# Optimization experiments

Measured on AMD Instinct MI355X. Metric: run time of the kernel, lower is better.

The kernel has to match this reference:

```python
import jax, jax.numpy as jnp
import numpy as np

B, S, D = 4, 4096, 2048

def setup_inputs() -> dict:
    key = jax.random.key(0)
    k1, k2 = jax.random.split(key)
    k = jax.random.normal(k1, (B, S, D), dtype=jnp.float32)
    v = jax.random.normal(k2, (B, S, D), dtype=jnp.float32)
    kv_state = jnp.zeros((D, D), dtype=jnp.float32)
    k_sum = jnp.zeros((D,), dtype=jnp.float32)
    return {"k": k, "v": v, "kv_state": kv_state, "k_sum": k_sum}

def reference(k, v, kv_state, k_sum):
    b, s, d = k.shape
    k_flat = k.reshape(-1, d)  # (N, D), N = B*S
    v_flat = v.reshape(-1, d)
    # Accumulate outer-product state: kv_state += sum_i k_i v_i^T
    kv_new = kv_state + jnp.einsum('nd,ne->de', k_flat, v_flat)
    ks_new = k_sum + k_flat.sum(axis=0)
    # Readout: context = k @ kv_state^T ; normalizer = k @ k_sum
    context = jnp.einsum('nd,ed->ne', k_flat, kv_new).reshape(b, s, d)
    normalizer = (k_flat @ ks_new).reshape(b, s, 1)
    return context, normalizer
```

## Files before the change

### kernel.cpp

```cpp
#include <hip/hip_runtime.h>
#include <hip/hip_bf16.h>
#include <cstdio>
#include <cstdint>

#define NBIG 16384
#define DDIM 2048
#define SPLITK 4

#define BM 256
#define BN 256
#define BKT 64

typedef __attribute__((ext_vector_type(4))) float f32x4;
typedef __attribute__((ext_vector_type(8))) short bf16x8;

__device__ __forceinline__ unsigned short f2bf(float f) {
  union { float f; unsigned u; } v; v.f = f;
  return (unsigned short)((v.u + 0x7FFFu + ((v.u >> 16) & 1u)) >> 16);
}

__device__ __forceinline__ void gll16(const void* g, void* l) {
  auto gp = reinterpret_cast<const __attribute__((address_space(1))) unsigned int*>(
      reinterpret_cast<uintptr_t>(g));
  auto lp = reinterpret_cast<__attribute__((address_space(3))) unsigned int*>(
      (unsigned int)reinterpret_cast<uintptr_t>(l));
  __builtin_amdgcn_global_load_lds(gp, lp, 16, 0, 0);
}

__device__ __forceinline__ void waitvm8() { asm volatile("s_waitcnt vmcnt(8)" ::: "memory"); }
__device__ __forceinline__ void waitvm0() { asm volatile("s_waitcnt vmcnt(0)" ::: "memory"); }
__device__ __forceinline__ void barrier_pinned() {
  __builtin_amdgcn_sched_barrier(0);
  __builtin_amdgcn_s_barrier();
  __builtin_amdgcn_sched_barrier(0);
}

__device__ __forceinline__ void xcd_swizzle(int& bx, int& by, int& bz) {
  const unsigned nx = gridDim.x, ny = gridDim.y;
  const unsigned nwg = nx * ny * gridDim.z;
  unsigned wg = blockIdx.x + nx * (blockIdx.y + ny * blockIdx.z);
  wg = (wg & 7u) * (nwg >> 3) + (wg >> 3);
  bx = wg % nx;
  unsigned r = wg / nx;
  by = r % ny;
  bz = r / ny;
}

__global__ __launch_bounds__(256) void prep_kernel(
    const float* __restrict__ k, const float* __restrict__ v,
    unsigned short* __restrict__ KT, unsigned short* __restrict__ VT,
    unsigned short* __restrict__ Kbf, float* __restrict__ ks)
{
  __shared__ unsigned short sm[64][66];
  __shared__ float sks[64];
  const int t = threadIdx.x;
  const int tiles_d = DDIM / 64;
  const int n0 = (blockIdx.x / tiles_d) * 64;
  const int d0 = (blockIdx.x % tiles_d) * 64;
  const bool is_k = (blockIdx.y == 0);
  const float* __restrict__ src = is_k ? k : v;
  unsigned short* __restrict__ dstT = is_k ? KT : VT;

  const int r = t >> 4;
  const int c = (t & 15) * 4;

  if (t < 64) sks[t] = 0.f;
  __syncthreads();

  float a0 = 0.f, a1 = 0.f, a2 = 0.f, a3 = 0.f;
#pragma unroll
  for (int i = 0; i < 4; ++i) {
    const int row = i * 16 + r;
    f32x4 val = *reinterpret_cast<const f32x4*>(&src[(size_t)(n0 + row) * DDIM + d0 + c]);
    unsigned short b0 = f2bf(val.x), b1 = f2bf(val.y), b2 = f2bf(val.z), b3 = f2bf(val.w);
    sm[row][c + 0] = b0; sm[row][c + 1] = b1;
    sm[row][c + 2] = b2; sm[row][c + 3] = b3;
    if (is_k) {
      unsigned int p0 = (unsigned)b0 | ((unsigned)b1 << 16);
      unsigned int p1 = (unsigned)b2 | ((unsigned)b3 << 16);
      *reinterpret_cast<uint2*>(&Kbf[(size_t)(n0 + row) * DDIM + d0 + c]) = make_uint2(p0, p1);
      a0 += val.x; a1 += val.y; a2 += val.z; a3 += val.w;
    }
  }
  if (is_k) {
    atomicAdd(&sks[c + 0], a0);
    atomicAdd(&sks[c + 1], a1);
    atomicAdd(&sks[c + 2], a2);
    atomicAdd(&sks[c + 3], a3);
  }
  __syncthreads();

#pragma unroll
  for (int i = 0; i < 4; ++i) {
    const int rowp = i * 16 + r;
    unsigned int p0 = (unsigned)sm[c + 0][rowp] | ((unsigned)sm[c + 1][rowp] << 16);
    unsigned int p1 = (unsigned)sm[c + 2][rowp] | ((unsigned)sm[c + 3][rowp] << 16);
    *reinterpret_cast<uint2*>(&dstT[(size_t)(d0 + rowp) * NBIG + n0 + c]) = make_uint2(p0, p1);
  }
  if (is_k && t < 64) atomicAdd(&ks[d0 + t], sks[t]);
}

__global__ void init_ks_kernel(const float* __restrict__ ksum, float* __restrict__ ks) {
  int i = blockIdx.x * 256 + threadIdx.x;
  if (i < DDIM) ks[i] = ksum[i];
}

template <bool BF16OUT>
__global__ __launch_bounds__(512, 2) void gemm256_kernel(
    const unsigned short* __restrict__ A, const unsigned short* __restrict__ B,
    void* __restrict__ Cv, int lda, int ldb, int kchunk, long long zstride)
{
  __shared__ unsigned short Abuf[2][BM * BKT];
  __shared__ unsigned short Bbuf[2][BN * BKT];

  int bx, by, bz;
  xcd_swizzle(bx, by, bz);

  const int t = threadIdx.x, lane = t & 63, w = t >> 6;
  const int wm = w >> 2, wn = w & 3;
  const int m0 = by * BM, n0 = bx * BN;
  const int kbeg = bz * kchunk;
  const int NT = kchunk / BKT;

  const int srow = lane >> 3;
  const int sgr  = (lane & 7) ^ srow;
  const unsigned short* Ag = A + (size_t)(m0 + srow) * lda + kbeg + sgr * 8;
  const unsigned short* Bg = B + (size_t)(n0 + srow) * ldb + kbeg + sgr * 8;

  const int hi = lane >> 4;
  const int lo7 = lane & 7;
  const int swz0 = ((0 + hi) ^ lo7) * 8;
  const int swz1 = ((4 + hi) ^ lo7) * 8;
  const int arow = (wm * 128 + (lane & 15)) * BKT;
  const int brow = (wn * 64 + (lane & 15)) * BKT;

  auto stage_op = [&](const unsigned short* G, unsigned short* Lbase, int ld_,
                      int kt, int half) {
    const unsigned short* g = G + (size_t)(half * 128 + w * 16) * ld_ + (size_t)kt * BKT;
    unsigned short* l = Lbase + (half * 128 + w * 16) * BKT;
    gll16(g, l);
    gll16(g + (size_t)8 * ld_, l + 8 * BKT);
  };

  stage_op(Bg, Bbuf[0], ldb, 0, 0); stage_op(Bg, Bbuf[0], ldb, 0, 1);
  stage_op(Ag, Abuf[0], lda, 0, 0); stage_op(Ag, Abuf[0], lda, 0, 1);
  stage_op(Bg, Bbuf[1], ldb, 1, 0); stage_op(Bg, Bbuf[1], ldb, 1, 1);
  stage_op(Ag, Abuf[1], lda, 1, 0); stage_op(Ag, Abuf[1], lda, 1, 1);
  waitvm8();
  __builtin_amdgcn_s_barrier();
  __builtin_amdgcn_sched_barrier(0);

  f32x4 acc[8][4] = {};

#pragma unroll 2
  for (int tl = 0; tl < NT; ++tl) {
    const int q = tl & 1;
    const unsigned short* Al = Abuf[q];
    const unsigned short* Bl = Bbuf[q];
    bf16x8 af[4][2], bA[2][2], bB[2][2];

#pragma unroll
    for (int m = 0; m < 4; ++m) {
      af[m][0] = *reinterpret_cast<const bf16x8*>(Al + arow + m * 16 * BKT + swz0);
      af[m][1] = *reinterpret_cast<const bf16x8*>(Al + arow + m * 16 * BKT + swz1);
    }
#pragma unroll
    for (int n = 0; n < 2; ++n) {
      bA[n][0] = *reinterpret_cast<const bf16x8*>(Bl + brow + n * 16 * BKT + swz0);
      bA[n][1] = *reinterpret_cast<const bf16x8*>(Bl + brow + n * 16 * BKT + swz1);
    }
    __builtin_amdgcn_s_setprio(1);
#pragma unroll
    for (int kk = 0; kk < 2; ++kk)
#pragma unroll
      for (int m = 0; m < 4; ++m)
#pragma unroll
        for (int n = 0; n < 2; ++n)
          acc[m][n] = __builtin_amdgcn_mfma_f32_16x16x32_bf16(af[m][kk], bA[n][kk], acc[m][n], 0, 0, 0);
    __builtin_amdgcn_s_setprio(0);

#pragma unroll
    for (int n = 0; n < 2; ++n) {
      bB[n][0] = *reinterpret_cast<const bf16x8*>(Bl + brow + (32 + n * 16) * BKT + swz0);
      bB[n][1] = *reinterpret_cast<const bf16x8*>(Bl + brow + (32 + n * 16) * BKT + swz1);
    }
    __builtin_amdgcn_s_setprio(1);
#pragma unroll
    for (int kk = 0; kk < 2; ++kk)
#pragma unroll
      for (int m = 0; m < 4; ++m)
#pragma unroll
        for (int n = 0; n < 2; ++n)
          acc[m][2 + n] = __builtin_amdgcn_mfma_f32_16x16x32_bf16(af[m][kk], bB[n][kk], acc[m][2 + n], 0, 0, 0);
    __builtin_amdgcn_s_setprio(0);
    barrier_pinned();

    if (tl + 2 < NT) {
      stage_op(Bg, Bbuf[q], ldb, tl + 2, 0);
      stage_op(Bg, Bbuf[q], ldb, tl + 2, 1);
    }
#pragma unroll
    for (int m = 0; m < 4; ++m) {
      af[m][0] = *reinterpret_cast<const bf16x8*>(Al + arow + (64 + m * 16) * BKT + swz0);
      af[m][1] = *reinterpret_cast<const bf16x8*>(Al + arow + (64 + m * 16) * BKT + swz1);
    }
    __builtin_amdgcn_s_setprio(1);
#pragma unroll
    for (int kk = 0; kk < 2; ++kk)
#pragma unroll
      for (int m = 0; m < 4; ++m)
#pragma unroll
        for (int n = 0; n < 2; ++n)
          acc[4 + m][n] = __builtin_amdgcn_mfma_f32_16x16x32_bf16(af[m][kk], bA[n][kk], acc[4 + m][n], 0, 0, 0);
    __builtin_amdgcn_s_setprio(0);
    barrier_pinned();

    if (tl + 2 < NT) {
      stage_op(Ag, Abuf[q], lda, tl + 2, 0);
      stage_op(Ag, Abuf[q], lda, tl + 2, 1);
    }
    __builtin_amdgcn_s_setprio(1);
#pragma unroll
    for (int kk = 0; kk < 2; ++kk)
#pragma unroll
      for (int m = 0; m < 4; ++m)
#pragma unroll
        for (int n = 0; n < 2; ++n)
          acc[4 + m][2 + n] = __builtin_amdgcn_mfma_f32_16x16x32_bf16(af[m][kk], bB[n][kk], acc[4 + m][2 + n], 0, 0, 0);
    __builtin_amdgcn_s_setprio(0);
    if (tl + 1 < NT) {
      if (tl + 2 < NT) waitvm8();
      else             waitvm0();
      __builtin_amdgcn_s_barrier();
      __builtin_amdgcn_sched_barrier(0);
    }
  }

  const int crow0 = m0 + wm * 128 + hi * 4;
  const int ccol0 = n0 + wn * 64 + (lane & 15);
  if (BF16OUT) {
    unsigned short* Cz = (unsigned short*)Cv + (size_t)bz * zstride;
#pragma unroll
    for (int m = 0; m < 8; ++m)
#pragma unroll
      for (int n = 0; n < 4; ++n)
#pragma unroll
        for (int j = 0; j < 4; ++j)
          Cz[(size_t)(crow0 + m * 16 + j) * DDIM + ccol0 + n * 16] = f2bf(acc[m][n][j]);
  } else {
    float* Cz = (float*)Cv + (size_t)bz * zstride;
#pragma unroll
    for (int m = 0; m < 8; ++m)
#pragma unroll
      for (int n = 0; n < 4; ++n)
#pragma unroll
        for (int j = 0; j < 4; ++j)
          Cz[(size_t)(crow0 + m * 16 + j) * DDIM + ccol0 + n * 16] = acc[m][n][j];
  }
}

__global__ __launch_bounds__(256) void kvconv_kernel(
    const unsigned short* __restrict__ kvp, const float* __restrict__ kvst,
    unsigned short* __restrict__ kvbf)
{
  size_t i = ((size_t)blockIdx.x * 256 + threadIdx.x) * 4;
  f32x4 s = *reinterpret_cast<const f32x4*>(&kvst[i]);
#pragma unroll
  for (int z = 0; z < SPLITK; ++z) {
    ushort4 p = *reinterpret_cast<const ushort4*>(&kvp[(size_t)z * DDIM * DDIM + i]);
    union { unsigned u; float f; } c0, c1, c2, c3;
    c0.u = (unsigned)p.x << 16; c1.u = (unsigned)p.y << 16;
    c2.u = (unsigned)p.z << 16; c3.u = (unsigned)p.w << 16;
    s.x += c0.f; s.y += c1.f; s.z += c2.f; s.w += c3.f;
  }
  unsigned int p0 = (unsigned)f2bf(s.x) | ((unsigned)f2bf(s.y) << 16);
  unsigned int p1 = (unsigned)f2bf(s.z) | ((unsigned)f2bf(s.w) << 16);
  *reinterpret_cast<uint2*>(&kvbf[i]) = make_uint2(p0, p1);
}

__global__ __launch_bounds__(256) void norm_kernel(
    const unsigned short* __restrict__ Kbf, const float* __restrict__ ks,
    float* __restrict__ out)
{
  const int lane = threadIdx.x & 63;
  const int w = threadIdx.x >> 6;
  const int row = blockIdx.x * 4 + w;
  const unsigned short* kr = Kbf + (size_t)row * DDIM;
  float s = 0.f;
#pragma unroll
  for (int i = 0; i < 4; ++i) {
    bf16x8 a = *reinterpret_cast<const bf16x8*>(&kr[i * 512 + lane * 8]);
    f32x4 b0 = *reinterpret_cast<const f32x4*>(&ks[i * 512 + lane * 8]);
    f32x4 b1 = *reinterpret_cast<const f32x4*>(&ks[i * 512 + lane * 8 + 4]);
    float af[8];
#pragma unroll
    for (int j = 0; j < 8; ++j) {
      union { unsigned u; float f; } cv;
      cv.u = ((unsigned)(unsigned short)a[j]) << 16;
      af[j] = cv.f;
    }
    s += af[0] * b0.x + af[1] * b0.y + af[2] * b0.z + af[3] * b0.w
       + af[4] * b1.x + af[5] * b1.y + af[6] * b1.z + af[7] * b1.w;
  }
  for (int off = 32; off; off >>= 1) s += __shfl_down(s, off, 64);
  if (lane == 0) out[row] = s;
}

extern "C" void kernel_launch(void* const* d_in, const int* in_sizes, int n_in,
                              void* d_out, int out_size, void* d_ws, size_t ws_size,
                              hipStream_t stream) {
  const float* k    = (const float*)d_in[0];
  const float* v    = (const float*)d_in[1];
  const float* kvst = (const float*)d_in[2];
  const float* ksum = (const float*)d_in[3];

  const size_t SZ_T = (size_t)DDIM * NBIG * 2;
  const size_t WS_NEED = SZ_T * 3 + (size_t)DDIM * DDIM * 2 + DDIM * 4;
  if (ws_size < WS_NEED) {
    fprintf(stderr, "kernel_launch: ws too small %zu < %zu\n", ws_size, WS_NEED);
    return;
  }
  char* ws = (char*)d_ws;
  unsigned short* KT   = (unsigned short*)ws;
  unsigned short* VT   = (unsigned short*)(ws + SZ_T);
  unsigned short* Kbf  = (unsigned short*)(ws + 2 * SZ_T);
  unsigned short* KVbf = (unsigned short*)(ws + 3 * SZ_T);
  float* ks            = (float*)(ws + 3 * SZ_T + (size_t)DDIM * DDIM * 2);

  float* ctx = (float*)d_out;
  float* nrm = ctx + (size_t)NBIG * DDIM;
  unsigned short* kvp = (unsigned short*)d_out;

  init_ks_kernel<<<(DDIM + 255) / 256, 256, 0, stream>>>(ksum, ks);
  prep_kernel<<<dim3((NBIG / 64) * (DDIM / 64), 2), 256, 0, stream>>>(k, v, KT, VT, Kbf, ks);
  gemm256_kernel<true><<<dim3(DDIM / BN, DDIM / BM, SPLITK), 512, 0, stream>>>(
      KT, VT, kvp, NBIG, NBIG, NBIG / SPLITK, (long long)DDIM * DDIM);
  kvconv_kernel<<<(DDIM * DDIM) / (256 * 4), 256, 0, stream>>>(kvp, kvst, KVbf);
  gemm256_kernel<false><<<dim3(DDIM / BN, NBIG / BM, 1), 512, 0, stream>>>(
      Kbf, KVbf, ctx, DDIM, DDIM, DDIM, 0);
  norm_kernel<<<NBIG / 4, 256, 0, stream>>>(Kbf, ks, nrm);
}
```

Measured before the change: 377.0 us.

## Restructure GEMM main loop into 8-phase ping-pong schedule with interleaved staged loads

Unrolls the K loop by two with explicit buffer indices and spreads the global-to-LDS staging of the next A and B tiles across the four MFMA phases. Each phase gets a barrier plus an lgkmcnt wait, and the vmcnt wait threshold drops to match the new number of outstanding loads. The goal is to overlap memory traffic with MFMA work more evenly and hide load latency. In exchange it adds many more barriers per tile, and the tighter wait counts risk synchronization stalls or races if they are wrong.

```diff
diff --git a/kernel.cpp b/kernel.cpp
--- a/kernel.cpp
+++ b/kernel.cpp
@@ -27,13 +27,10 @@
   __builtin_amdgcn_global_load_lds(gp, lp, 16, 0, 0);
 }
 
-__device__ __forceinline__ void waitvm8() { asm volatile("s_waitcnt vmcnt(8)" ::: "memory"); }
+__device__ __forceinline__ void waitvm4() { asm volatile("s_waitcnt vmcnt(4)" ::: "memory"); }
 __device__ __forceinline__ void waitvm0() { asm volatile("s_waitcnt vmcnt(0)" ::: "memory"); }
-__device__ __forceinline__ void barrier_pinned() {
-  __builtin_amdgcn_sched_barrier(0);
-  __builtin_amdgcn_s_barrier();
-  __builtin_amdgcn_sched_barrier(0);
-}
+__device__ __forceinline__ void waitlgkm0() { asm volatile("s_waitcnt lgkmcnt(0)" ::: "memory"); }
+#define SB0 __builtin_amdgcn_sched_barrier(0)
 
 __device__ __forceinline__ void xcd_swizzle(int& bx, int& by, int& bz) {
   const unsigned nx = gridDim.x, ny = gridDim.y;
@@ -145,96 +142,185 @@
   stage_op(Bg, Bbuf[0], ldb, 0, 0); stage_op(Bg, Bbuf[0], ldb, 0, 1);
   stage_op(Ag, Abuf[0], lda, 0, 0); stage_op(Ag, Abuf[0], lda, 0, 1);
   stage_op(Bg, Bbuf[1], ldb, 1, 0); stage_op(Bg, Bbuf[1], ldb, 1, 1);
-  stage_op(Ag, Abuf[1], lda, 1, 0); stage_op(Ag, Abuf[1], lda, 1, 1);
-  waitvm8();
+  waitvm4();
   __builtin_amdgcn_s_barrier();
-  __builtin_amdgcn_sched_barrier(0);
+  SB0;
 
   f32x4 acc[8][4] = {};
-
-#pragma unroll 2
-  for (int tl = 0; tl < NT; ++tl) {
-    const int q = tl & 1;
-    const unsigned short* Al = Abuf[q];
-    const unsigned short* Bl = Bbuf[q];
+  const int NI = NT / 2;
+
+#pragma unroll 1
+  for (int it = 0; it < NI; ++it) {
+    const int T = it * 2;
+    const bool pf2 = (T + 2 < NT);
+    const bool pf3 = (T + 3 < NT);
+    const bool last = (it == NI - 1);
     bf16x8 af[4][2], bA[2][2], bB[2][2];
 
-#pragma unroll
-    for (int m = 0; m < 4; ++m) {
-      af[m][0] = *reinterpret_cast<const bf16x8*>(Al + arow + m * 16 * BKT + swz0);
-      af[m][1] = *reinterpret_cast<const bf16x8*>(Al + arow + m * 16 * BKT + swz1);
+    {
+      const unsigned short* Al = Abuf[0];
+      const unsigned short* Bl = Bbuf[0];
+
+      stage_op(Ag, Abuf[1], lda, T + 1, 0);
+#pragma unroll
+      for (int m = 0; m < 4; ++m) {
+        af[m][0] = *reinterpret_cast<const bf16x8*>(Al + arow + m * 16 * BKT + swz0);
+        af[m][1] = *reinterpret_cast<const bf16x8*>(Al + arow + m * 16 * BKT + swz1);
+      }
+#pragma unroll
+      for (int n = 0; n < 2; ++n) {
+        bA[n][0] = *reinterpret_cast<const bf16x8*>(Bl + brow + n * 16 * BKT + swz0);
+        bA[n][1] = *reinterpret_cast<const bf16x8*>(Bl + brow + n * 16 * BKT + swz1);
+      }
+      SB0; __builtin_amdgcn_s_barrier(); waitlgkm0(); SB0;
+      __builtin_amdgcn_s_setprio(1);
+#pragma unroll
+      for (int kk = 0; kk < 2; ++kk)
+#pragma unroll
+        for (int m = 0; m < 4; ++m)
+#pragma unroll
+          for (int n = 0; n < 2; ++n)
+            acc[m][n] = __builtin_amdgcn_mfma_f32_16x16x32_bf16(af[m][kk], bA[n][kk], acc[m][n], 0, 0, 0);
+      __builtin_amdgcn_s_setprio(0);
+      SB0; __builtin_amdgcn_s_barrier(); SB0;
+
+      stage_op(Ag, Abuf[1], lda, T + 1, 1);
+#pragma unroll
+      for (int n = 0; n < 2; ++n) {
+        bB[n][0] = *reinterpret_cast<const bf16x8*>(Bl + brow + (32 + n * 16) * BKT + swz0);
+        bB[n][1] = *reinterpret_cast<const bf16x8*>(Bl + brow + (32 + n * 16) * BKT + swz1);
+      }
+      SB0; __builtin_amdgcn_s_barrier(); waitlgkm0(); SB0;
+      __builtin_amdgcn_s_setprio(1);
+#pragma unroll
+      for (int kk = 0; kk < 2; ++kk)
+#pragma unroll
+        for (int m = 0; m < 4; ++m)
+#pragma unroll
+          for (int n = 0; n < 2; ++n)
+            acc[m][2 + n] = __builtin_amdgcn_mfma_f32_16x16x32_bf16(af[m][kk], bB[n][kk], acc[m][2 + n], 0, 0, 0);
+      __builtin_amdgcn_s_setprio(0);
+      SB0; __builtin_amdgcn_s_barrier(); SB0;
+
+      if (pf2) stage_op(Bg, Bbuf[0], ldb, T + 2, 0);
+#pragma unroll
+      for (int m = 0; m < 4; ++m) {
+        af[m][0] = *reinterpret_cast<const bf16x8*>(Al + arow + (64 + m * 16) * BKT + swz0);
+        af[m][1] = *reinterpret_cast<const bf16x8*>(Al + arow + (64 + m * 16) * BKT + swz1);
+      }
+      SB0; __builtin_amdgcn_s_barrier(); waitlgkm0(); SB0;
+      __builtin_amdgcn_s_setprio(1);
+#pragma unroll
+      for (int kk = 0; kk < 2; ++kk)
+#pragma unroll
+        for (int m = 0; m < 4; ++m)
+#pragma unroll
+          for (int n = 0; n < 2; ++n)
+            acc[4 + m][n] = __builtin_amdgcn_mfma_f32_16x16x32_bf16(af[m][kk], bA[n][kk], acc[4 + m][n], 0, 0, 0);
+      __builtin_amdgcn_s_setprio(0);
+      SB0; __builtin_amdgcn_s_barrier(); SB0;
+
+      if (pf2) stage_op(Bg, Bbuf[0], ldb, T + 2, 1);
+      SB0; __builtin_amdgcn_s_barrier(); SB0;
+      __builtin_amdgcn_s_setprio(1);
+#pragma unroll
+      for (int kk = 0; kk < 2; ++kk)
+#pragma unroll
+        for (int m = 0; m < 4; ++m)
+#pragma unroll
+          for (int n = 0; n < 2; ++n)
+            acc[4 + m][2 + n] = __builtin_amdgcn_mfma_f32_16x16x32_bf16(af[m][kk], bB[n][kk], acc[4 + m][2 + n], 0, 0, 0);
+      __builtin_amdgcn_s_setprio(0);
+      SB0;
+      if (last) waitvm0();
+      else      waitvm4();
+      __builtin_amdgcn_s_barrier();
+      SB0;
     }
-#pragma unroll
-    for (int n = 0; n < 2; ++n) {
-      bA[n][0] = *reinterpret_cast<const bf16x8*>(Bl + brow + n * 16 * BKT + swz0);
-      bA[n][1] = *reinterpret_cast<const bf16x8*>(Bl + brow + n * 16 * BKT + swz1);
+
+    {
+      const unsigned short* Al = Abuf[1];
+      const unsigned short* Bl = Bbuf[1];
+
+      if (pf2) stage_op(Ag, Abuf[0], lda, T + 2, 0);
+#pragma unroll
+      for (int m = 0; m < 4; ++m) {
+        af[m][0] = *reinterpret_cast<const bf16x8*>(Al + arow + m * 16 * BKT + swz0);
+        af[m][1] = *reinterpret_cast<const bf16x8*>(Al + arow + m * 16 * BKT + swz1);
+      }
+#pragma unroll
+      for (int n = 0; n < 2; ++n) {
+        bA[n][0] = *reinterpret_cast<const bf16x8*>(Bl + brow + n * 16 * BKT + swz0);
+        bA[n][1] = *reinterpret_cast<const bf16x8*>(Bl + brow + n * 16 * BKT + swz1);
+      }
+      SB0; __builtin_amdgcn_s_barrier(); waitlgkm0(); SB0;
+      __builtin_amdgcn_s_setprio(1);
+#pragma unroll
+      for (int kk = 0; kk < 2; ++kk)
+#pragma unroll
+        for (int m = 0; m < 4; ++m)
+#pragma unroll
+          for (int n = 0; n < 2; ++n)
+            acc[m][n] = __builtin_amdgcn_mfma_f32_16x16x32_bf16(af[m][kk], bA[n][kk], acc[m][n], 0, 0, 0);
+      __builtin_amdgcn_s_setprio(0);
+      SB0; __builtin_amdgcn_s_barrier(); SB0;
+
+      if (pf2) stage_op(Ag, Abuf[0], lda, T + 2, 1);
+#pragma unroll
+      for (int n = 0; n < 2; ++n) {
+        bB[n][0] = *reinterpret_cast<const bf16x8*>(Bl + brow + (32 + n * 16) * BKT + swz0);
+        bB[n][1] = *reinterpret_cast<const bf16x8*>(Bl + brow + (32 + n * 16) * BKT + swz1);
+      }
+      SB0; __builtin_amdgcn_s_barrier(); waitlgkm0(); SB0;
+      __builtin_amdgcn_s_setprio(1);
+#pragma unroll
+      for (int kk = 0; kk < 2; ++kk)
+#pragma unroll
+        for (int m = 0; m < 4; ++m)
+#pragma unroll
+          for (int n = 0; n < 2; ++n)
+            acc[m][2 + n] = __builtin_amdgcn_mfma_f32_16x16x32_bf16(af[m][kk], bB[n][kk], acc[m][2 + n], 0, 0, 0);
+      __builtin_amdgcn_s_setprio(0);
+      SB0; __builtin_amdgcn_s_barrier(); SB0;
+
+      if (pf3) stage_op(Bg, Bbuf[1], ldb, T + 3, 0);
+#pragma unroll
+      for (int m = 0; m < 4; ++m) {
+        af[m][0] = *reinterpret_cast<const bf16x8*>(Al + arow + (64 + m * 16) * BKT + swz0);
+        af[m][1] = *reinterpret_cast<const bf16x8*>(Al + arow + (64 + m * 16) * BKT + swz1);
+      }
+      SB0; __builtin_amdgcn_s_barrier(); waitlgkm0(); SB0;
+      __builtin_amdgcn_s_setprio(1);
+#pragma unroll
+      for (int kk = 0; kk < 2; ++kk)
+#pragma unroll
+        for (int m = 0; m < 4; ++m)
+#pragma unroll
+          for (int n = 0; n < 2; ++n)
+            acc[4 + m][n] = __builtin_amdgcn_mfma_f32_16x16x32_bf16(af[m][kk], bA[n][kk], acc[4 + m][n], 0, 0, 0);
+      __builtin_amdgcn_s_setprio(0);
+      SB0; __builtin_amdgcn_s_barrier(); SB0;
+
+      if (pf3) stage_op(Bg, Bbuf[1], ldb, T + 3, 1);
+      SB0; __builtin_amdgcn_s_barrier(); SB0;
+      __builtin_amdgcn_s_setprio(1);
+#pragma unroll
+      for (int kk = 0; kk < 2; ++kk)
+#pragma unroll
+        for (int m = 0; m < 4; ++m)
+#pragma unroll
+          for (int n = 0; n < 2; ++n)
+            acc[4 + m][2 + n] = __builtin_amdgcn_mfma_f32_16x16x32_bf16(af[m][kk], bB[n][kk], acc[4 + m][2 + n], 0, 0, 0);
+      __builtin_amdgcn_s_setprio(0);
+      SB0;
+      if (!last) {
+        waitvm4();
+        __builtin_amdgcn_s_barrier();
+        SB0;
+      }
     }
-    __builtin_amdgcn_s_setprio(1);
-#pragma unroll
-    for (int kk = 0; kk < 2; ++kk)
-#pragma unroll
-      for (int m = 0; m < 4; ++m)
-#pragma unroll
-        for (int n = 0; n < 2; ++n)
-          acc[m][n] = __builtin_amdgcn_mfma_f32_16x16x32_bf16(af[m][kk], bA[n][kk], acc[m][n], 0, 0, 0);
-    __builtin_amdgcn_s_setprio(0);
-
-#pragma unroll
-    for (int n = 0; n < 2; ++n) {
-      bB[n][0] = *reinterpret_cast<const bf16x8*>(Bl + brow + (32 + n * 16) * BKT + swz0);
-      bB[n][1] = *reinterpret_cast<const bf16x8*>(Bl + brow + (32 + n * 16) * BKT + swz1);
-    }
-    __builtin_amdgcn_s_setprio(1);
-#pragma unroll
-    for (int kk = 0; kk < 2; ++kk)
-#pragma unroll
-      for (int m = 0; m < 4; ++m)
-#pragma unroll
-        for (int n = 0; n < 2; ++n)
-          acc[m][2 + n] = __builtin_amdgcn_mfma_f32_16x16x32_bf16(af[m][kk], bB[n][kk], acc[m][2 + n], 0, 0, 0);
-    __builtin_amdgcn_s_setprio(0);
-    barrier_pinned();
-
-    if (tl + 2 < NT) {
-      stage_op(Bg, Bbuf[q], ldb, tl + 2, 0);
-      stage_op(Bg, Bbuf[q], ldb, tl + 2, 1);
-    }
-#pragma unroll
-    for (int m = 0; m < 4; ++m) {
-      af[m][0] = *reinterpret_cast<const bf16x8*>(Al + arow + (64 + m * 16) * BKT + swz0);
-      af[m][1] = *reinterpret_cast<const bf16x8*>(Al + arow + (64 + m * 16) * BKT + swz1);
-    }
-    __builtin_amdgcn_s_setprio(1);
-#pragma unroll
-    for (int kk = 0; kk < 2; ++kk)
-#pragma unroll
-      for (int m = 0; m < 4; ++m)
-#pragma unroll
-        for (int n = 0; n < 2; ++n)
-          acc[4 + m][n] = __builtin_amdgcn_mfma_f32_16x16x32_bf16(af[m][kk], bA[n][kk], acc[4 + m][n], 0, 0, 0);
-    __builtin_amdgcn_s_setprio(0);
-    barrier_pinned();
-
-    if (tl + 2 < NT) {
-      stage_op(Ag, Abuf[q], lda, tl + 2, 0);
-      stage_op(Ag, Abuf[q], lda, tl + 2, 1);
-    }
-    __builtin_amdgcn_s_setprio(1);
-#pragma unroll
-    for (int kk = 0; kk < 2; ++kk)
-#pragma unroll
-      for (int m = 0; m < 4; ++m)
-#pragma unroll
-        for (int n = 0; n < 2; ++n)
-          acc[4 + m][2 + n] = __builtin_amdgcn_mfma_f32_16x16x32_bf16(af[m][kk], bB[n][kk], acc[4 + m][2 + n], 0, 0, 0);
-    __builtin_amdgcn_s_setprio(0);
-    if (tl + 1 < NT) {
-      if (tl + 2 < NT) waitvm8();
-      else             waitvm0();
-      __builtin_amdgcn_s_barrier();
-      __builtin_amdgcn_sched_barrier(0);
-    }
-  }
+  }
+  waitvm0();
 
   const int crow0 = m0 + wm * 128 + hi * 4;
   const int ccol0 = n0 + wn * 64 + (lane & 15);
```

New measurement: 374.7 us. Within noise of the previous version (-0.6%).
